# Kernel tuning notes

Measured on AMD Instinct MI355X. Metric: run time of the kernel, lower is better.

Reference implementation:

```python
import jax, jax.numpy as jnp
import numpy as np

D_MODEL = 4096
NUM_EXPERTS = 64
TOP_K = 2


def setup_inputs() -> dict:
    key = jax.random.key(0)
    k1, k2 = jax.random.split(key)
    hidden_states = jax.random.normal(k1, (4, 4096, D_MODEL), dtype=jnp.float32)
    # nn.Linear(d_model, num_experts, bias=False) weight: [num_experts, d_model]
    W = jax.random.normal(k2, (NUM_EXPERTS, D_MODEL), dtype=jnp.float32) * (1.0 / np.sqrt(D_MODEL))
    return {"hidden_states": hidden_states, "W": W}


def reference(hidden_states, W):
    # router_logits: [B, S, E]
    router_logits = jnp.einsum("bsd,ed->bse", hidden_states, W)
    # top-k over experts (torch.topk returns values sorted descending; lax.top_k matches)
    top_k_logits, top_k_indices = jax.lax.top_k(router_logits, TOP_K)
    routing_weights = jax.nn.softmax(top_k_logits, axis=-1)
    return routing_weights, top_k_indices
```

## Files before the change

kernel.cpp:

```cpp
#include <hip/hip_runtime.h>
#include <stdint.h>

#define D_MODEL 4096
#define N_EXP   64
#define N_TOK   16384
#define MTILE   64
#define KC      64
#define NCHUNK  (D_MODEL / KC)

typedef float  f32x4  __attribute__((ext_vector_type(4)));
typedef short  bf16x8 __attribute__((ext_vector_type(8)));

__device__ __forceinline__ void cvt8(float4 v0, float4 v1, uint4& hp, uint4& lp) {
  float f[8] = {v0.x, v0.y, v0.z, v0.w, v1.x, v1.y, v1.z, v1.w};
  unsigned hb[8], lb[8];
#pragma unroll
  for (int i = 0; i < 8; ++i) {
    unsigned u = __builtin_bit_cast(unsigned, f[i]);
    unsigned r = u + 0x7FFFu + ((u >> 16) & 1u);
    unsigned h = r & 0xFFFF0000u;
    float    res = f[i] - __builtin_bit_cast(float, h);
    lb[i] = __builtin_bit_cast(unsigned, res);
    hb[i] = h;
  }
  hp.x = (hb[0] >> 16) | hb[1];
  hp.y = (hb[2] >> 16) | hb[3];
  hp.z = (hb[4] >> 16) | hb[5];
  hp.w = (hb[6] >> 16) | hb[7];
  lp.x = (lb[0] >> 16) | (lb[1] & 0xFFFF0000u);
  lp.y = (lb[2] >> 16) | (lb[3] & 0xFFFF0000u);
  lp.z = (lb[4] >> 16) | (lb[5] & 0xFFFF0000u);
  lp.w = (lb[6] >> 16) | (lb[7] & 0xFFFF0000u);
}

__device__ __forceinline__ void* lds_slot(void* buf, int row, int kb) {
  return (void*)((char*)buf + ((((row) << 3) + ((kb) ^ ((row) & 7))) << 4));
}

__global__ __launch_bounds__(256) void SimpleMoERouter_54219667144993_kernel(
    const float* __restrict__ X, const float* __restrict__ W,
    float* __restrict__ outw, float* __restrict__ outi)
{
  __shared__ short sAh[MTILE * KC];
  __shared__ short sAl[MTILE * KC];
  __shared__ short sWh[N_EXP * KC];
  __shared__ short sWl[N_EXP * KC];
  __shared__ float sLog[MTILE * 65];

  const int tid  = threadIdx.x;
  const int lane = tid & 63;
  const int wv   = tid >> 6;
  const int tok0 = blockIdx.x * MTILE;

  const int srow = tid >> 3;
  const int skb  = tid & 7;

  const float* gA0 = X + (size_t)(tok0 + srow) * D_MODEL + skb * 8;
  const float* gA1 = gA0 + (size_t)32 * D_MODEL;
  const float* gW0 = W + (size_t)srow * D_MODEL + skb * 8;
  const float* gW1 = gW0 + (size_t)32 * D_MODEL;

  float4 st[8];

  auto LOAD = [&](int it) {
    const int off = it * KC;
    st[0] = *(const float4*)(gA0 + off);
    st[1] = *(const float4*)(gA0 + off + 4);
    st[2] = *(const float4*)(gA1 + off);
    st[3] = *(const float4*)(gA1 + off + 4);
    st[4] = *(const float4*)(gW0 + off);
    st[5] = *(const float4*)(gW0 + off + 4);
    st[6] = *(const float4*)(gW1 + off);
    st[7] = *(const float4*)(gW1 + off + 4);
  };

  auto STORE = [&]() {
    uint4 hp, lp;
    cvt8(st[0], st[1], hp, lp);
    *(uint4*)lds_slot(sAh, srow, skb) = hp;
    *(uint4*)lds_slot(sAl, srow, skb) = lp;
    cvt8(st[2], st[3], hp, lp);
    *(uint4*)lds_slot(sAh, srow + 32, skb) = hp;
    *(uint4*)lds_slot(sAl, srow + 32, skb) = lp;
    cvt8(st[4], st[5], hp, lp);
    *(uint4*)lds_slot(sWh, srow, skb) = hp;
    *(uint4*)lds_slot(sWl, srow, skb) = lp;
    cvt8(st[6], st[7], hp, lp);
    *(uint4*)lds_slot(sWh, srow + 32, skb) = hp;
    *(uint4*)lds_slot(sWl, srow + 32, skb) = lp;
  };

  f32x4 acc[4] = {{0.f,0.f,0.f,0.f},{0.f,0.f,0.f,0.f},
                  {0.f,0.f,0.f,0.f},{0.f,0.f,0.f,0.f}};

  const int arow = wv * 16 + (lane & 15);
  const int kq   = lane >> 4;

  LOAD(0);
  STORE();
  __syncthreads();

  for (int it = 0; it < NCHUNK; ++it) {
    if (it + 1 < NCHUNK) LOAD(it + 1);
#pragma unroll
    for (int h = 0; h < 2; ++h) {
      const int kb = h * 4 + kq;
      bf16x8 ah = *(const bf16x8*)lds_slot(sAh, arow, kb);
      bf16x8 al = *(const bf16x8*)lds_slot(sAl, arow, kb);
#pragma unroll
      for (int nt = 0; nt < 4; ++nt) {
        const int brow = nt * 16 + (lane & 15);
        bf16x8 bh = *(const bf16x8*)lds_slot(sWh, brow, kb);
        bf16x8 bl = *(const bf16x8*)lds_slot(sWl, brow, kb);
        acc[nt] = __builtin_amdgcn_mfma_f32_16x16x32_bf16(ah, bh, acc[nt], 0, 0, 0);
        acc[nt] = __builtin_amdgcn_mfma_f32_16x16x32_bf16(ah, bl, acc[nt], 0, 0, 0);
        acc[nt] = __builtin_amdgcn_mfma_f32_16x16x32_bf16(al, bh, acc[nt], 0, 0, 0);
      }
    }
    __syncthreads();
    if (it + 1 < NCHUNK) {
      STORE();
      __syncthreads();
    }
  }

#pragma unroll
  for (int nt = 0; nt < 4; ++nt) {
#pragma unroll
    for (int r = 0; r < 4; ++r) {
      const int trow = wv * 16 + (lane >> 4) * 4 + r;
      const int e    = nt * 16 + (lane & 15);
      sLog[trow * 65 + e] = acc[nt][r];
    }
  }
  __syncthreads();

  if (tid < MTILE) {
    float best = -3.4e38f, sec = -3.4e38f;
    int bi = 0, si = 0;
#pragma unroll 8
    for (int e = 0; e < N_EXP; ++e) {
      const float v  = sLog[tid * 65 + e];
      const bool b1 = v > best;
      const bool b2 = v > sec;
      sec  = b1 ? best : (b2 ? v : sec);
      si   = b1 ? bi   : (b2 ? e : si);
      best = b1 ? v : best;
      bi   = b1 ? e : bi;
    }
    const float ed  = expf(sec - best);
    const float inv = 1.0f / (1.0f + ed);
    const int gt = tok0 + tid;
    outw[2 * gt]     = inv;
    outw[2 * gt + 1] = ed * inv;
    outi[2 * gt]     = (float)bi;
    outi[2 * gt + 1] = (float)si;
  }
}

extern "C" void kernel_launch(void* const* d_in, const int* in_sizes, int n_in,
                              void* d_out, int out_size, void* d_ws, size_t ws_size,
                              hipStream_t stream) {
  const float* X = (const float*)d_in[0];
  const float* W = (const float*)d_in[1];
  float* outw = (float*)d_out;
  float* outi = (float*)d_out + (size_t)N_TOK * 2;
  hipLaunchKernelGGL(SimpleMoERouter_54219667144993_kernel,
                     dim3(N_TOK / MTILE), dim3(256), 0, stream,
                     X, W, outw, outi);
}
```

Baseline: 403.0 us.

## Split K across waves with register-direct loads, dropping LDS staging

Each block now covers 16 tokens instead of 64, and the four waves split the 4096-long K dimension into quarters. Partial logits are reduced through shared memory before the top-2 selection. Both X and W fragments are loaded straight from global memory into registers and converted to bf16 hi/lo there, which removes the LDS staging and the per-chunk barriers. In exchange, W is now re-read and re-converted by every block, four times as many blocks as before, so there is much more W traffic through L2 and more conversion ALU work.

```diff
diff --git a/kernel.cpp b/kernel.cpp
--- a/kernel.cpp
+++ b/kernel.cpp
@@ -1,136 +1,80 @@
 #include <hip/hip_runtime.h>
 #include <stdint.h>
 
-#define D_MODEL 4096
-#define N_EXP   64
-#define N_TOK   16384
-#define MTILE   64
-#define KC      64
-#define NCHUNK  (D_MODEL / KC)
+#define D_MODEL  4096
+#define N_EXP    64
+#define N_TOK    16384
+#define MTILE    16
+#define KSTEP    32
+#define KQ       1024
+#define NSTEP    (KQ / KSTEP)
 
 typedef float  f32x4  __attribute__((ext_vector_type(4)));
 typedef short  bf16x8 __attribute__((ext_vector_type(8)));
 
-__device__ __forceinline__ void cvt8(float4 v0, float4 v1, uint4& hp, uint4& lp) {
+__device__ __forceinline__ void cvt8(float4 v0, float4 v1, bf16x8& hi, bf16x8& lo) {
   float f[8] = {v0.x, v0.y, v0.z, v0.w, v1.x, v1.y, v1.z, v1.w};
-  unsigned hb[8], lb[8];
 #pragma unroll
   for (int i = 0; i < 8; ++i) {
-    unsigned u = __builtin_bit_cast(unsigned, f[i]);
-    unsigned r = u + 0x7FFFu + ((u >> 16) & 1u);
-    unsigned h = r & 0xFFFF0000u;
-    float    res = f[i] - __builtin_bit_cast(float, h);
-    lb[i] = __builtin_bit_cast(unsigned, res);
-    hb[i] = h;
+    unsigned u  = __builtin_bit_cast(unsigned, f[i]);
+    unsigned r  = u + 0x7FFFu + ((u >> 16) & 1u);
+    unsigned hb = r & 0xFFFF0000u;
+    float    res = f[i] - __builtin_bit_cast(float, hb);
+    hi[i] = (short)(hb >> 16);
+    lo[i] = (short)(__builtin_bit_cast(unsigned, res) >> 16);
   }
-  hp.x = (hb[0] >> 16) | hb[1];
-  hp.y = (hb[2] >> 16) | hb[3];
-  hp.z = (hb[4] >> 16) | hb[5];
-  hp.w = (hb[6] >> 16) | hb[7];
-  lp.x = (lb[0] >> 16) | (lb[1] & 0xFFFF0000u);
-  lp.y = (lb[2] >> 16) | (lb[3] & 0xFFFF0000u);
-  lp.z = (lb[4] >> 16) | (lb[5] & 0xFFFF0000u);
-  lp.w = (lb[6] >> 16) | (lb[7] & 0xFFFF0000u);
-}
-
-__device__ __forceinline__ void* lds_slot(void* buf, int row, int kb) {
-  return (void*)((char*)buf + ((((row) << 3) + ((kb) ^ ((row) & 7))) << 4));
 }
 
 __global__ __launch_bounds__(256) void SimpleMoERouter_54219667144993_kernel(
     const float* __restrict__ X, const float* __restrict__ W,
     float* __restrict__ outw, float* __restrict__ outi)
 {
-  __shared__ short sAh[MTILE * KC];
-  __shared__ short sAl[MTILE * KC];
-  __shared__ short sWh[N_EXP * KC];
-  __shared__ short sWl[N_EXP * KC];
-  __shared__ float sLog[MTILE * 65];
+  __shared__ float sRed[4][MTILE][N_EXP + 4];
 
   const int tid  = threadIdx.x;
   const int lane = tid & 63;
   const int wv   = tid >> 6;
   const int tok0 = blockIdx.x * MTILE;
+  const int r16  = lane & 15;
+  const int kq   = lane >> 4;
 
-  const int srow = tid >> 3;
-  const int skb  = tid & 7;
-
-  const float* gA0 = X + (size_t)(tok0 + srow) * D_MODEL + skb * 8;
-  const float* gA1 = gA0 + (size_t)32 * D_MODEL;
-  const float* gW0 = W + (size_t)srow * D_MODEL + skb * 8;
-  const float* gW1 = gW0 + (size_t)32 * D_MODEL;
-
-  float4 st[8];
-
-  auto LOAD = [&](int it) {
-    const int off = it * KC;
-    st[0] = *(const float4*)(gA0 + off);
-    st[1] = *(const float4*)(gA0 + off + 4);
-    st[2] = *(const float4*)(gA1 + off);
-    st[3] = *(const float4*)(gA1 + off + 4);
-    st[4] = *(const float4*)(gW0 + off);
-    st[5] = *(const float4*)(gW0 + off + 4);
-    st[6] = *(const float4*)(gW1 + off);
-    st[7] = *(const float4*)(gW1 + off + 4);
-  };
-
-  auto STORE = [&]() {
-    uint4 hp, lp;
-    cvt8(st[0], st[1], hp, lp);
-    *(uint4*)lds_slot(sAh, srow, skb) = hp;
-    *(uint4*)lds_slot(sAl, srow, skb) = lp;
-    cvt8(st[2], st[3], hp, lp);
-    *(uint4*)lds_slot(sAh, srow + 32, skb) = hp;
-    *(uint4*)lds_slot(sAl, srow + 32, skb) = lp;
-    cvt8(st[4], st[5], hp, lp);
-    *(uint4*)lds_slot(sWh, srow, skb) = hp;
-    *(uint4*)lds_slot(sWl, srow, skb) = lp;
-    cvt8(st[6], st[7], hp, lp);
-    *(uint4*)lds_slot(sWh, srow + 32, skb) = hp;
-    *(uint4*)lds_slot(sWl, srow + 32, skb) = lp;
-  };
+  const float* xp = X + (size_t)(tok0 + r16) * D_MODEL + wv * KQ + kq * 8;
+  const float* wp = W + (size_t)r16 * D_MODEL + wv * KQ + kq * 8;
 
   f32x4 acc[4] = {{0.f,0.f,0.f,0.f},{0.f,0.f,0.f,0.f},
                   {0.f,0.f,0.f,0.f},{0.f,0.f,0.f,0.f}};
 
-  const int arow = wv * 16 + (lane & 15);
-  const int kq   = lane >> 4;
+  float4 xa = *(const float4*)xp;
+  float4 xb = *(const float4*)(xp + 4);
 
-  LOAD(0);
-  STORE();
-  __syncthreads();
-
-  for (int it = 0; it < NCHUNK; ++it) {
-    if (it + 1 < NCHUNK) LOAD(it + 1);
+  for (int s = 0; s < NSTEP; ++s) {
+    const int off = s * KSTEP;
+    float4 nxa, nxb;
+    if (s + 1 < NSTEP) {
+      nxa = *(const float4*)(xp + off + KSTEP);
+      nxb = *(const float4*)(xp + off + KSTEP + 4);
+    }
+    bf16x8 ah, al;
+    cvt8(xa, xb, ah, al);
 #pragma unroll
-    for (int h = 0; h < 2; ++h) {
-      const int kb = h * 4 + kq;
-      bf16x8 ah = *(const bf16x8*)lds_slot(sAh, arow, kb);
-      bf16x8 al = *(const bf16x8*)lds_slot(sAl, arow, kb);
-#pragma unroll
-      for (int nt = 0; nt < 4; ++nt) {
-        const int brow = nt * 16 + (lane & 15);
-        bf16x8 bh = *(const bf16x8*)lds_slot(sWh, brow, kb);
-        bf16x8 bl = *(const bf16x8*)lds_slot(sWl, brow, kb);
-        acc[nt] = __builtin_amdgcn_mfma_f32_16x16x32_bf16(ah, bh, acc[nt], 0, 0, 0);
-        acc[nt] = __builtin_amdgcn_mfma_f32_16x16x32_bf16(ah, bl, acc[nt], 0, 0, 0);
-        acc[nt] = __builtin_amdgcn_mfma_f32_16x16x32_bf16(al, bh, acc[nt], 0, 0, 0);
-      }
+    for (int nt = 0; nt < 4; ++nt) {
+      const float* wq = wp + (size_t)(nt * 16) * D_MODEL + off;
+      float4 wa = *(const float4*)wq;
+      float4 wb = *(const float4*)(wq + 4);
+      bf16x8 bh, bl;
+      cvt8(wa, wb, bh, bl);
+      acc[nt] = __builtin_amdgcn_mfma_f32_16x16x32_bf16(ah, bh, acc[nt], 0, 0, 0);
+      acc[nt] = __builtin_amdgcn_mfma_f32_16x16x32_bf16(ah, bl, acc[nt], 0, 0, 0);
+      acc[nt] = __builtin_amdgcn_mfma_f32_16x16x32_bf16(al, bh, acc[nt], 0, 0, 0);
     }
-    __syncthreads();
-    if (it + 1 < NCHUNK) {
-      STORE();
-      __syncthreads();
-    }
+    xa = nxa; xb = nxb;
   }
 
 #pragma unroll
   for (int nt = 0; nt < 4; ++nt) {
 #pragma unroll
     for (int r = 0; r < 4; ++r) {
-      const int trow = wv * 16 + (lane >> 4) * 4 + r;
-      const int e    = nt * 16 + (lane & 15);
-      sLog[trow * 65 + e] = acc[nt][r];
+      sRed[wv][kq * 4 + r][nt * 16 + r16] = acc[nt][r];
     }
   }
   __syncthreads();
@@ -140,7 +84,8 @@
     int bi = 0, si = 0;
 #pragma unroll 8
     for (int e = 0; e < N_EXP; ++e) {
-      const float v  = sLog[tid * 65 + e];
+      const float v = sRed[0][tid][e] + sRed[1][tid][e]
+                    + sRed[2][tid][e] + sRed[3][tid][e];
       const bool b1 = v > best;
       const bool b2 = v > sec;
       sec  = b1 ? best : (b2 ? v : sec);
```

Measured after the change: 428.9 us. +6.4%, slower.
